# Performance work log

Measured on AMD Instinct MI355X. Metric: run time of the kernel, lower is better.

## Reference

```python
import jax, jax.numpy as jnp
import numpy as np

D_MODEL = 1024
N_HEADS = 16
D_HEAD = D_MODEL // N_HEADS


def setup_inputs() -> dict:
    key = jax.random.key(0)
    k1, k2, k3 = jax.random.split(key, 3)
    B, T = 2, 2048
    x = jax.random.normal(k1, (B, T, D_MODEL), dtype=jnp.float32)
    # kaiming_normal fan_out on torch Linear weight [out, in]: std = sqrt(2/out)
    qkv_w = jax.random.normal(k2, (3 * D_MODEL, D_MODEL), dtype=jnp.float32) * np.sqrt(2.0 / (3 * D_MODEL)).astype(np.float32)
    out_w = jax.random.normal(k3, (D_MODEL, D_MODEL), dtype=jnp.float32) * np.sqrt(2.0 / D_MODEL).astype(np.float32)
    return {"x": x, "qkv_w": qkv_w, "out_w": out_w}


def rotate_half(x):
    x1, x2 = x[..., : x.shape[-1] // 2], x[..., x.shape[-1] // 2 :]
    return jnp.concatenate((-x2, x1), axis=-1)


def reference(x, qkv_w, out_w):
    B, T, D = x.shape
    H, dh = N_HEADS, D_HEAD
    scale = dh ** -0.5

    qkv = jnp.einsum('btd,ed->bte', x, qkv_w)  # [B,T,3D]
    q, k, v = jnp.split(qkv, 3, axis=-1)
    # [B,H,T,dh]
    q = q.reshape(B, T, H, dh).transpose(0, 2, 1, 3)
    k = k.reshape(B, T, H, dh).transpose(0, 2, 1, 3)
    v = v.reshape(B, T, H, dh).transpose(0, 2, 1, 3)

    # rotary embeddings
    inv_freq = 1.0 / (10000.0 ** (jnp.arange(0, dh, 2, dtype=jnp.float32) / dh))
    t = jnp.arange(T, dtype=jnp.float32)
    freqs = jnp.einsum('i,j->ij', t, inv_freq)        # [T, dh/2]
    emb = jnp.concatenate((freqs, freqs), axis=-1)    # [T, dh]
    cos = jnp.cos(emb)[None, None]                    # [1,1,T,dh]
    sin = jnp.sin(emb)[None, None]
    q = q * cos + rotate_half(q) * sin
    k = k * cos + rotate_half(k) * sin

    scores = jnp.einsum('bhqd,bhkd->bhqk', q, k) * scale
    causal = jnp.tril(jnp.ones((T, T), dtype=bool))
    scores = jnp.where(causal, scores, -jnp.inf)
    attn = jax.nn.softmax(scores, axis=-1)
    out = jnp.einsum('bhqk,bhkd->bhqd', attn, v)      # [B,H,T,dh]
    out = out.transpose(0, 2, 1, 3).reshape(B, T, D)
    return jnp.einsum('btd,ed->bte', out, out_w)
```

## Files before the change

kernel.cpp:

```cpp
#include <hip/hip_runtime.h>
#include <hip/hip_bf16.h>
#include <cmath>

#define Bb   2
#define Tseq 2048
#define NH   16
#define DM   1024

using f32x4 = __attribute__((ext_vector_type(4))) float;
using s16x8 = __attribute__((ext_vector_type(8))) short;

typedef const __attribute__((address_space(1))) unsigned char* as1p;
typedef __attribute__((address_space(3))) unsigned char* as3p;

static __device__ __forceinline__ void gload_lds16(const void* g, void* l){
  __builtin_amdgcn_global_load_lds((as1p)g, (as3p)l, 16, 0, 0);
}

static __device__ __forceinline__ float b2f(unsigned short u){
  union { unsigned int u; float f; } v; v.u = ((unsigned int)u) << 16; return v.f;
}
static __device__ __forceinline__ unsigned short f2b(float f){
  union { float f; unsigned int u; } v; v.f = f;
  unsigned int u = v.u;
  return (unsigned short)((u + 0x7fffu + ((u >> 16) & 1u)) >> 16);
}

__global__ void k_convert(const float* __restrict__ in, unsigned short* __restrict__ out, int n){
  int stride = gridDim.x * blockDim.x;
  for (int i = blockIdx.x * blockDim.x + threadIdx.x; i * 4 < n; i += stride) {
    const float4 v = *reinterpret_cast<const float4*>(in + (size_t)i * 4);
    ushort4 o; o.x = f2b(v.x); o.y = f2b(v.y); o.z = f2b(v.z); o.w = f2b(v.w);
    *reinterpret_cast<ushort4*>(out + (size_t)i * 4) = o;
  }
}

__global__ void k_tables(float* __restrict__ cosT, float* __restrict__ sinT){
  int idx = blockIdx.x * blockDim.x + threadIdx.x;
  int t = idx >> 5, j = idx & 31;
  double invf = pow(10000.0, -(double)j / 32.0);
  double a = (double)t * invf;
  cosT[idx] = (float)cos(a);
  sinT[idx] = (float)sin(a);
}

template<int OUT_BF16>
__global__ __launch_bounds__(256) void k_gemm_bt(const unsigned short* __restrict__ A,
                                                 const unsigned short* __restrict__ W,
                                                 void* __restrict__ Cout,
                                                 int M, int N, int K){
  __shared__ unsigned short As[128*32];
  __shared__ unsigned short Bs[128*32];
  const int bm = blockIdx.x * 128, bn = blockIdx.y * 128;
  const int tid = threadIdx.x;
  const int lane = tid & 63, w = tid >> 6;
  const int wr = w >> 1, wc = w & 1;
  const int g = lane >> 4, ln = lane & 15;
  f32x4 acc[4][4] = {};
  char* asb = (char*)As + w * 2048;
  char* bsb = (char*)Bs + w * 2048;
  const int lrow = lane >> 2;
  const int kcol = (lane & 3) * 8;
  const size_t aro = (size_t)(bm + w * 32 + lrow) * K;
  const size_t bro = (size_t)(bn + w * 32 + lrow) * K;
  for (int k0 = 0; k0 < K; k0 += 32) {
    gload_lds16(A + aro + k0 + kcol,                  asb);
    gload_lds16(A + aro + (size_t)16 * K + k0 + kcol, asb + 1024);
    gload_lds16(W + bro + k0 + kcol,                  bsb);
    gload_lds16(W + bro + (size_t)16 * K + k0 + kcol, bsb + 1024);
    __syncthreads();
    s16x8 af[4], bfr[4];
    #pragma unroll
    for (int mt = 0; mt < 4; ++mt)
      af[mt] = *reinterpret_cast<const s16x8*>(&As[(wr*64 + mt*16 + ln)*32 + g*8]);
    #pragma unroll
    for (int nt = 0; nt < 4; ++nt)
      bfr[nt] = *reinterpret_cast<const s16x8*>(&Bs[(wc*64 + nt*16 + ln)*32 + g*8]);
    #pragma unroll
    for (int mt = 0; mt < 4; ++mt)
      #pragma unroll
      for (int nt = 0; nt < 4; ++nt)
        acc[mt][nt] = __builtin_amdgcn_mfma_f32_16x16x32_bf16(af[mt], bfr[nt], acc[mt][nt], 0, 0, 0);
    __syncthreads();
  }
  #pragma unroll
  for (int mt = 0; mt < 4; ++mt)
    #pragma unroll
    for (int nt = 0; nt < 4; ++nt)
      #pragma unroll
      for (int r = 0; r < 4; ++r) {
        int row = bm + wr*64 + mt*16 + g*4 + r;
        int col = bn + wc*64 + nt*16 + ln;
        float vv = acc[mt][nt][r];
        if (OUT_BF16) reinterpret_cast<unsigned short*>(Cout)[(size_t)row * N + col] = f2b(vv);
        else          reinterpret_cast<float*>(Cout)[(size_t)row * N + col] = vv;
      }
}

__global__ __launch_bounds__(256) void k_rope_split(const unsigned short* __restrict__ qkv,
                                                    const float* __restrict__ cosT,
                                                    const float* __restrict__ sinT,
                                                    unsigned short* __restrict__ qr,
                                                    unsigned short* __restrict__ kr){
  int bt = blockIdx.x;
  int b = bt / Tseq, t = bt % Tseq;
  const unsigned short* row = qkv + (size_t)bt * 3072;
  for (int d = threadIdx.x; d < 1024; d += 256) {
    int h = d >> 6, dd = d & 63;
    int j = dd & 31;
    float c = cosT[t*32 + j], s = sinT[t*32 + j];
    int part = (dd < 32) ? (d + 32) : (d - 32);
    float xq  = b2f(row[d]);
    float xq2 = b2f(row[part]);
    float qv = (dd < 32) ? (xq*c - xq2*s) : (xq*c + xq2*s);
    size_t head_off = ((size_t)(b*NH + h) * Tseq + t) * 64 + dd;
    qr[head_off] = f2b(qv * 0.125f);
    float xk  = b2f(row[1024 + d]);
    float xk2 = b2f(row[1024 + part]);
    float kv = (dd < 32) ? (xk*c - xk2*s) : (xk*c + xk2*s);
    kr[head_off] = f2b(kv);
  }
}

__global__ __launch_bounds__(256) void k_vtrans(const unsigned short* __restrict__ qkv,
                                                unsigned short* __restrict__ vt){
  __shared__ unsigned short L[64*72];
  const int blk = blockIdx.x;
  const int tt64 = blk & 31, bh = blk >> 5;
  const int b = bh >> 4, h = bh & 15;
  const int t0 = tt64 * 64;
  const int tid = threadIdx.x;
  {
    const int tr = tid >> 2, c = tid & 3;
    const unsigned short* src = qkv + ((size_t)(b * Tseq) + t0 + tr) * 3072 + 2048 + h * 64 + c * 16;
    uint4 a0 = *reinterpret_cast<const uint4*>(src);
    uint4 a1 = *reinterpret_cast<const uint4*>(src + 8);
    *reinterpret_cast<uint4*>(&L[tr * 72 + c * 16])     = a0;
    *reinterpret_cast<uint4*>(&L[tr * 72 + c * 16 + 8]) = a1;
  }
  __syncthreads();
  {
    const int d = tid >> 2, c = tid & 3;
    unsigned int wq[8];
    #pragma unroll
    for (int j = 0; j < 8; ++j) {
      unsigned int lo = L[(c * 16 + 2 * j)     * 72 + d];
      unsigned int hi = L[(c * 16 + 2 * j + 1) * 72 + d];
      wq[j] = lo | (hi << 16);
    }
    unsigned short* dst = vt + ((size_t)bh * 64 + d) * Tseq + t0 + c * 16;
    *reinterpret_cast<uint4*>(dst)     = make_uint4(wq[0], wq[1], wq[2], wq[3]);
    *reinterpret_cast<uint4*>(dst + 8) = make_uint4(wq[4], wq[5], wq[6], wq[7]);
  }
}

__global__ __launch_bounds__(512, 2) void k_attn(const unsigned short* __restrict__ Qr,
                                                 const unsigned short* __restrict__ Kr,
                                                 const unsigned short* __restrict__ Vt,
                                                 unsigned short* __restrict__ Ao){
  __shared__ unsigned short Ks[64*64];
  __shared__ unsigned short Vs[64*64];
  __shared__ unsigned short Ps[8][16*72];
  const int blk = (int)blockIdx.x;
  const int pj = blk & 7;
  const int bh = blk >> 3;
  const unsigned short* Q  = Qr + (size_t)bh * Tseq * 64;
  const unsigned short* Kp = Kr + (size_t)bh * Tseq * 64;
  const unsigned short* Vp = Vt + (size_t)bh * 64 * Tseq;
  const int tid = threadIdx.x;
  const int w = tid >> 6, lane = tid & 63;
  const int g = lane >> 4, ln = lane & 15;
  const int srow = tid >> 3, scol = (tid & 7) * 8;
  const int wb = srow * 128 + ((scol * 2) ^ ((srow & 7) << 4));
  const int x0 = (g * 16)      ^ ((ln & 7) << 4);
  const int x1 = (64 + g * 16) ^ ((ln & 7) << 4);
  unsigned short* Pw = Ps[w];
  const int b = bh / NH, h = bh % NH;

  #pragma unroll
  for (int pass = 0; pass < 2; ++pass) {
    const int j = pass ? (15 - pj) : pj;
    const int q0 = j * 128;
    const int ntiles = 2 * j + 2;
    const int q0w = q0 + w * 16;

    s16x8 qf0 = *reinterpret_cast<const s16x8*>(&Q[(size_t)(q0w + ln) * 64 + g * 8]);
    s16x8 qf1 = *reinterpret_cast<const s16x8*>(&Q[(size_t)(q0w + ln) * 64 + 32 + g * 8]);

    f32x4 oacc[4] = {};
    float lsum = 0.f;

    __syncthreads();
    {
      uint4 kv = *reinterpret_cast<const uint4*>(&Kp[(size_t)srow * 64 + scol]);
      uint4 vv = *reinterpret_cast<const uint4*>(&Vp[(size_t)srow * Tseq + scol]);
      *reinterpret_cast<uint4*>((char*)Ks + wb) = kv;
      *reinterpret_cast<uint4*>((char*)Vs + wb) = vv;
    }
    __syncthreads();

    for (int kt = 0; kt < ntiles; ++kt) {
      const bool pre = (kt < ntiles - 1);
      uint4 nk, nv;
      if (pre) {
        nk = *reinterpret_cast<const uint4*>(&Kp[(size_t)((kt + 1) * 64 + srow) * 64 + scol]);
        nv = *reinterpret_cast<const uint4*>(&Vp[(size_t)srow * Tseq + (kt + 1) * 64 + scol]);
      }
      f32x4 s[4] = {};
      const char* kb = (const char*)Ks;
      __builtin_amdgcn_s_setprio(1);
      #pragma unroll
      for (int nt = 0; nt < 4; ++nt) {
        s16x8 kfa = *reinterpret_cast<const s16x8*>(kb + nt * 2048 + ln * 128 + x0);
        s16x8 kfb = *reinterpret_cast<const s16x8*>(kb + nt * 2048 + ln * 128 + x1);
        s[nt] = __builtin_amdgcn_mfma_f32_16x16x32_bf16(kfa, qf0, s[nt], 0, 0, 0);
        s[nt] = __builtin_amdgcn_mfma_f32_16x16x32_bf16(kfb, qf1, s[nt], 0, 0, 0);
      }
      __builtin_amdgcn_s_setprio(0);
      if (kt >= ntiles - 2) {
        const int kb0 = (kt - (ntiles - 2)) * 64;
        #pragma unroll
        for (int nt = 0; nt < 4; ++nt)
          #pragma unroll
          for (int r = 0; r < 4; ++r)
            if (kb0 + nt * 16 + g * 4 + r > w * 16 + ln) s[nt][r] = -1e30f;
      }
      #pragma unroll
      for (int nt = 0; nt < 4; ++nt)
        #pragma unroll
        for (int r = 0; r < 4; ++r) {
          float p = __expf(s[nt][r]);
          s[nt][r] = p;
          lsum += p;
        }
      #pragma unroll
      for (int nt = 0; nt < 4; ++nt) {
        unsigned int lo = (unsigned int)f2b(s[nt][0]) | ((unsigned int)f2b(s[nt][1]) << 16);
        unsigned int hi = (unsigned int)f2b(s[nt][2]) | ((unsigned int)f2b(s[nt][3]) << 16);
        *reinterpret_cast<uint2*>(&Pw[ln * 72 + nt * 16 + g * 4]) = make_uint2(lo, hi);
      }
      asm volatile("s_waitcnt lgkmcnt(0)" ::: "memory");
      __builtin_amdgcn_sched_barrier(0);
      s16x8 pf0 = *reinterpret_cast<const s16x8*>(&Pw[ln * 72 + g * 8]);
      s16x8 pf1 = *reinterpret_cast<const s16x8*>(&Pw[ln * 72 + 32 + g * 8]);
      const char* vb = (const char*)Vs;
      __builtin_amdgcn_s_setprio(1);
      #pragma unroll
      for (int nt = 0; nt < 4; ++nt) {
        s16x8 vfa = *reinterpret_cast<const s16x8*>(vb + nt * 2048 + ln * 128 + x0);
        s16x8 vfb = *reinterpret_cast<const s16x8*>(vb + nt * 2048 + ln * 128 + x1);
        oacc[nt] = __builtin_amdgcn_mfma_f32_16x16x32_bf16(vfa, pf0, oacc[nt], 0, 0, 0);
        oacc[nt] = __builtin_amdgcn_mfma_f32_16x16x32_bf16(vfb, pf1, oacc[nt], 0, 0, 0);
      }
      __builtin_amdgcn_s_setprio(0);
      __syncthreads();
      if (pre) {
        *reinterpret_cast<uint4*>((char*)Ks + wb) = nk;
        *reinterpret_cast<uint4*>((char*)Vs + wb) = nv;
        __syncthreads();
      }
    }

    float l = lsum;
    l += __shfl_xor(l, 16);
    l += __shfl_xor(l, 32);
    float inv = 1.f / l;
    #pragma unroll
    for (int nt = 0; nt < 4; ++nt) {
      unsigned int lo = (unsigned int)f2b(oacc[nt][0] * inv) | ((unsigned int)f2b(oacc[nt][1] * inv) << 16);
      unsigned int hi = (unsigned int)f2b(oacc[nt][2] * inv) | ((unsigned int)f2b(oacc[nt][3] * inv) << 16);
      *reinterpret_cast<uint2*>(&Pw[ln * 72 + nt * 16 + g * 4]) = make_uint2(lo, hi);
    }
    asm volatile("s_waitcnt lgkmcnt(0)" ::: "memory");
    __builtin_amdgcn_sched_barrier(0);
    const int rr = lane >> 2;
    const int cc = (lane & 3) * 8;
    uint4 ov0 = *reinterpret_cast<const uint4*>(&Pw[rr * 72 + cc]);
    uint4 ov1 = *reinterpret_cast<const uint4*>(&Pw[rr * 72 + cc + 32]);
    int t = q0w + rr;
    unsigned short* orow = &Ao[((size_t)(b * Tseq + t) * DM) + h * 64];
    *reinterpret_cast<uint4*>(orow + cc)      = ov0;
    *reinterpret_cast<uint4*>(orow + cc + 32) = ov1;
  }
}

extern "C" void kernel_launch(void* const* d_in, const int* in_sizes, int n_in,
                              void* d_out, int out_size, void* d_ws, size_t ws_size,
                              hipStream_t stream) {
  const float* x    = (const float*)d_in[0];
  const float* qkvw = (const float*)d_in[1];
  const float* outw = (const float*)d_in[2];
  float* out = (float*)d_out;
  char* ws = (char*)d_ws;
  size_t off = 0;
  auto alloc = [&](size_t bytes)->void*{ void* p = ws + off; off += (bytes + 255) & ~(size_t)255; return p; };
  unsigned short* x_bf   = (unsigned short*)alloc((size_t)Bb*Tseq*DM*2);
  unsigned short* qw_bf  = (unsigned short*)alloc((size_t)3*DM*DM*2);
  unsigned short* ow_bf  = (unsigned short*)alloc((size_t)DM*DM*2);
  float*          cosT   = (float*)alloc((size_t)Tseq*32*4);
  float*          sinT   = (float*)alloc((size_t)Tseq*32*4);
  unsigned short* qkv_bf = (unsigned short*)alloc((size_t)Bb*Tseq*3*DM*2);
  unsigned short* qr     = (unsigned short*)alloc((size_t)Bb*NH*Tseq*64*2);
  unsigned short* kr     = (unsigned short*)alloc((size_t)Bb*NH*Tseq*64*2);
  unsigned short* vt     = (unsigned short*)alloc((size_t)Bb*NH*Tseq*64*2);
  unsigned short* ao     = (unsigned short*)alloc((size_t)Bb*Tseq*DM*2);
  (void)ws_size; (void)in_sizes; (void)n_in; (void)out_size;

  const int nx  = Bb*Tseq*DM;
  const int nqw = 3*DM*DM;
  const int now = DM*DM;
  k_convert<<<2048, 256, 0, stream>>>(x, x_bf, nx);
  k_convert<<<2048, 256, 0, stream>>>(qkvw, qw_bf, nqw);
  k_convert<<<1024, 256, 0, stream>>>(outw, ow_bf, now);
  k_tables<<<256, 256, 0, stream>>>(cosT, sinT);
  k_gemm_bt<1><<<dim3(32, 24), 256, 0, stream>>>(x_bf, qw_bf, qkv_bf, Bb*Tseq, 3*DM, DM);
  k_rope_split<<<Bb*Tseq, 256, 0, stream>>>(qkv_bf, cosT, sinT, qr, kr);
  k_vtrans<<<Bb*NH*(Tseq/64), 256, 0, stream>>>(qkv_bf, vt);
  k_attn<<<dim3(Bb*NH*8), 512, 0, stream>>>(qr, kr, vt, ao);
  k_gemm_bt<0><<<dim3(32, 8), 256, 0, stream>>>(ao, ow_bf, out, Bb*Tseq, DM, DM);
}
```

Baseline: 128.9 us.

## Double-buffer K/V tiles, keep P in registers via 16x16x16 MFMA, shrink attention blocks

The attention kernel moves from 512-thread blocks with 128-query tiles to 256-thread blocks with 64-query tiles, launching twice as many blocks. K/V tiles are double-buffered in shared memory, which removes one barrier per iteration. The P matrix is no longer staged through shared memory: the probabilities are packed into registers and fed straight into 16x16x16 bf16 MFMAs whose operand layout matches the score accumulator. The cost is twice as many, smaller MFMAs for the PV product, plus double the LDS for K/V.

```diff
diff --git a/kernel.cpp b/kernel.cpp
--- a/kernel.cpp
+++ b/kernel.cpp
@@ -9,6 +9,7 @@
 
 using f32x4 = __attribute__((ext_vector_type(4))) float;
 using s16x8 = __attribute__((ext_vector_type(8))) short;
+using s16x4 = __attribute__((ext_vector_type(4))) short;
 
 typedef const __attribute__((address_space(1))) unsigned char* as1p;
 typedef __attribute__((address_space(3))) unsigned char* as3p;
@@ -16,6 +17,15 @@
 static __device__ __forceinline__ void gload_lds16(const void* g, void* l){
   __builtin_amdgcn_global_load_lds((as1p)g, (as3p)l, 16, 0, 0);
 }
+
+#if defined(__has_builtin)
+#if __has_builtin(__builtin_amdgcn_mfma_f32_16x16x16bf16_1k)
+#define MFMA16(acc, va, pb) (acc) = __builtin_amdgcn_mfma_f32_16x16x16bf16_1k((va), (pb), (acc), 0, 0, 0)
+#endif
+#endif
+#ifndef MFMA16
+#define MFMA16(acc, va, pb) asm volatile("s_nop 1\n\tv_mfma_f32_16x16x16_bf16 %0, %1, %2, %0" : "+v"(acc) : "v"(va), "v"(pb))
+#endif
 
 static __device__ __forceinline__ float b2f(unsigned short u){
   union { unsigned int u; float f; } v; v.u = ((unsigned int)u) << 16; return v.f;
@@ -154,24 +164,27 @@
   }
 }
 
-__global__ __launch_bounds__(512, 2) void k_attn(const unsigned short* __restrict__ Qr,
+__global__ __launch_bounds__(256, 2) void k_attn(const unsigned short* __restrict__ Qr,
                                                  const unsigned short* __restrict__ Kr,
                                                  const unsigned short* __restrict__ Vt,
                                                  unsigned short* __restrict__ Ao){
-  __shared__ unsigned short Ks[64*64];
-  __shared__ unsigned short Vs[64*64];
-  __shared__ unsigned short Ps[8][16*72];
+  __shared__ unsigned short Ks[2][64*64];
+  __shared__ unsigned short Vs[2][64*64];
+  __shared__ unsigned short Ps[4][16*72];
   const int blk = (int)blockIdx.x;
-  const int pj = blk & 7;
-  const int bh = blk >> 3;
+  const int pj = blk & 15;
+  const int bh = blk >> 4;
   const unsigned short* Q  = Qr + (size_t)bh * Tseq * 64;
   const unsigned short* Kp = Kr + (size_t)bh * Tseq * 64;
   const unsigned short* Vp = Vt + (size_t)bh * 64 * Tseq;
   const int tid = threadIdx.x;
   const int w = tid >> 6, lane = tid & 63;
   const int g = lane >> 4, ln = lane & 15;
-  const int srow = tid >> 3, scol = (tid & 7) * 8;
-  const int wb = srow * 128 + ((scol * 2) ^ ((srow & 7) << 4));
+  const int srow = tid >> 2;
+  const int c2 = (tid & 3) * 2;
+  const int wb0 = srow * 128 + ((c2 * 16)        ^ ((srow & 7) << 4));
+  const int wb1 = srow * 128 + ((c2 * 16 + 16)   ^ ((srow & 7) << 4));
+  const int scol = c2 * 8;
   const int x0 = (g * 16)      ^ ((ln & 7) << 4);
   const int x1 = (64 + g * 16) ^ ((ln & 7) << 4);
   unsigned short* Pw = Ps[w];
@@ -179,9 +192,9 @@
 
   #pragma unroll
   for (int pass = 0; pass < 2; ++pass) {
-    const int j = pass ? (15 - pj) : pj;
-    const int q0 = j * 128;
-    const int ntiles = 2 * j + 2;
+    const int j = pass ? (31 - pj) : pj;
+    const int q0 = j * 64;
+    const int ntiles = j + 1;
     const int q0w = q0 + w * 16;
 
     s16x8 qf0 = *reinterpret_cast<const s16x8*>(&Q[(size_t)(q0w + ln) * 64 + g * 8]);
@@ -190,24 +203,32 @@
     f32x4 oacc[4] = {};
     float lsum = 0.f;
 
-    __syncthreads();
     {
-      uint4 kv = *reinterpret_cast<const uint4*>(&Kp[(size_t)srow * 64 + scol]);
-      uint4 vv = *reinterpret_cast<const uint4*>(&Vp[(size_t)srow * Tseq + scol]);
-      *reinterpret_cast<uint4*>((char*)Ks + wb) = kv;
-      *reinterpret_cast<uint4*>((char*)Vs + wb) = vv;
+      uint4 k0 = *reinterpret_cast<const uint4*>(&Kp[(size_t)srow * 64 + scol]);
+      uint4 k1 = *reinterpret_cast<const uint4*>(&Kp[(size_t)srow * 64 + scol + 8]);
+      uint4 v0 = *reinterpret_cast<const uint4*>(&Vp[(size_t)srow * Tseq + scol]);
+      uint4 v1 = *reinterpret_cast<const uint4*>(&Vp[(size_t)srow * Tseq + scol + 8]);
+      *reinterpret_cast<uint4*>((char*)Ks[0] + wb0) = k0;
+      *reinterpret_cast<uint4*>((char*)Ks[0] + wb1) = k1;
+      *reinterpret_cast<uint4*>((char*)Vs[0] + wb0) = v0;
+      *reinterpret_cast<uint4*>((char*)Vs[0] + wb1) = v1;
     }
     __syncthreads();
+    int cur = 0;
 
     for (int kt = 0; kt < ntiles; ++kt) {
-      const bool pre = (kt < ntiles - 1);
-      uint4 nk, nv;
+      const bool pre = (kt + 1 < ntiles);
+      uint4 nk0, nk1, nv0, nv1;
       if (pre) {
-        nk = *reinterpret_cast<const uint4*>(&Kp[(size_t)((kt + 1) * 64 + srow) * 64 + scol]);
-        nv = *reinterpret_cast<const uint4*>(&Vp[(size_t)srow * Tseq + (kt + 1) * 64 + scol]);
+        const unsigned short* gk = &Kp[(size_t)((kt + 1) * 64 + srow) * 64 + scol];
+        const unsigned short* gv = &Vp[(size_t)srow * Tseq + (kt + 1) * 64 + scol];
+        nk0 = *reinterpret_cast<const uint4*>(gk);
+        nk1 = *reinterpret_cast<const uint4*>(gk + 8);
+        nv0 = *reinterpret_cast<const uint4*>(gv);
+        nv1 = *reinterpret_cast<const uint4*>(gv + 8);
       }
       f32x4 s[4] = {};
-      const char* kb = (const char*)Ks;
+      const char* kb = (const char*)Ks[cur];
       __builtin_amdgcn_s_setprio(1);
       #pragma unroll
       for (int nt = 0; nt < 4; ++nt) {
@@ -217,48 +238,42 @@
         s[nt] = __builtin_amdgcn_mfma_f32_16x16x32_bf16(kfb, qf1, s[nt], 0, 0, 0);
       }
       __builtin_amdgcn_s_setprio(0);
-      if (kt >= ntiles - 2) {
-        const int kb0 = (kt - (ntiles - 2)) * 64;
+      if (kt == ntiles - 1) {
         #pragma unroll
         for (int nt = 0; nt < 4; ++nt)
           #pragma unroll
           for (int r = 0; r < 4; ++r)
-            if (kb0 + nt * 16 + g * 4 + r > w * 16 + ln) s[nt][r] = -1e30f;
-      }
+            if (nt * 16 + g * 4 + r > w * 16 + ln) s[nt][r] = -1e30f;
+      }
+      s16x4 pb[4];
       #pragma unroll
       for (int nt = 0; nt < 4; ++nt)
         #pragma unroll
         for (int r = 0; r < 4; ++r) {
           float p = __expf(s[nt][r]);
-          s[nt][r] = p;
           lsum += p;
+          pb[nt][r] = (short)f2b(p);
         }
-      #pragma unroll
-      for (int nt = 0; nt < 4; ++nt) {
-        unsigned int lo = (unsigned int)f2b(s[nt][0]) | ((unsigned int)f2b(s[nt][1]) << 16);
-        unsigned int hi = (unsigned int)f2b(s[nt][2]) | ((unsigned int)f2b(s[nt][3]) << 16);
-        *reinterpret_cast<uint2*>(&Pw[ln * 72 + nt * 16 + g * 4]) = make_uint2(lo, hi);
-      }
-      asm volatile("s_waitcnt lgkmcnt(0)" ::: "memory");
-      __builtin_amdgcn_sched_barrier(0);
-      s16x8 pf0 = *reinterpret_cast<const s16x8*>(&Pw[ln * 72 + g * 8]);
-      s16x8 pf1 = *reinterpret_cast<const s16x8*>(&Pw[ln * 72 + 32 + g * 8]);
-      const char* vb = (const char*)Vs;
+      const char* vb = (const char*)Vs[cur];
       __builtin_amdgcn_s_setprio(1);
       #pragma unroll
-      for (int nt = 0; nt < 4; ++nt) {
-        s16x8 vfa = *reinterpret_cast<const s16x8*>(vb + nt * 2048 + ln * 128 + x0);
-        s16x8 vfb = *reinterpret_cast<const s16x8*>(vb + nt * 2048 + ln * 128 + x1);
-        oacc[nt] = __builtin_amdgcn_mfma_f32_16x16x32_bf16(vfa, pf0, oacc[nt], 0, 0, 0);
-        oacc[nt] = __builtin_amdgcn_mfma_f32_16x16x32_bf16(vfb, pf1, oacc[nt], 0, 0, 0);
+      for (int dt = 0; dt < 4; ++dt) {
+        #pragma unroll
+        for (int nt = 0; nt < 4; ++nt) {
+          s16x4 va = *reinterpret_cast<const s16x4*>(vb + (dt * 16 + ln) * 128 + ((nt * 32 + g * 8) ^ ((ln & 7) << 4)));
+          MFMA16(oacc[dt], va, pb[nt]);
+        }
       }
       __builtin_amdgcn_s_setprio(0);
+      if (pre) {
+        const int nxt = cur ^ 1;
+        *reinterpret_cast<uint4*>((char*)Ks[nxt] + wb0) = nk0;
+        *reinterpret_cast<uint4*>((char*)Ks[nxt] + wb1) = nk1;
+        *reinterpret_cast<uint4*>((char*)Vs[nxt] + wb0) = nv0;
+        *reinterpret_cast<uint4*>((char*)Vs[nxt] + wb1) = nv1;
+      }
       __syncthreads();
-      if (pre) {
-        *reinterpret_cast<uint4*>((char*)Ks + wb) = nk;
-        *reinterpret_cast<uint4*>((char*)Vs + wb) = nv;
-        __syncthreads();
-      }
+      cur ^= 1;
     }
 
     float l = lsum;
@@ -316,6 +331,6 @@
   k_gemm_bt<1><<<dim3(32, 24), 256, 0, stream>>>(x_bf, qw_bf, qkv_bf, Bb*Tseq, 3*DM, DM);
   k_rope_split<<<Bb*Tseq, 256, 0, stream>>>(qkv_bf, cosT, sinT, qr, kr);
   k_vtrans<<<Bb*NH*(Tseq/64), 256, 0, stream>>>(qkv_bf, vt);
-  k_attn<<<dim3(Bb*NH*8), 512, 0, stream>>>(qr, kr, vt, ao);
+  k_attn<<<dim3(Bb*NH*16), 256, 0, stream>>>(qr, kr, vt, ao);
   k_gemm_bt<0><<<dim3(32, 8), 256, 0, stream>>>(ao, ow_bf, out, Bb*Tseq, DM, DM);
 }
```

After: 134.8 us. +4.5%, slower.
